# Performance work log

Measured on AMD Instinct MI355X. Metric: run time of the kernel, lower is better.

## Reference

```python
import jax, jax.numpy as jnp
import numpy as np

PAGE = 16  # page_size hard-coded in the torch module's forward


def setup_inputs() -> dict:
    rng = np.random.default_rng(0)
    B = 4096
    pre = rng.integers(0, 4096, size=B).astype(np.int32)
    ext = rng.integers(1, 8192, size=B).astype(np.int32)
    seq = (pre + ext).astype(np.int32)
    # last token slot of the existing prefix (identity layout); -1 when pre==0
    # (kernel never reads it in that case since num_part1 == 0).
    last_loc = (pre - 1).astype(np.int32)
    free_page = rng.permutation(2_097_152).astype(np.int32)
    return {
        "pre_lens": jnp.asarray(pre),
        "seq_lens": jnp.asarray(seq),
        "last_loc": jnp.asarray(last_loc),
        "free_page": jnp.asarray(free_page),
    }


def reference(pre_lens, seq_lens, last_loc, free_page):
    ext = seq_lens - pre_lens                      # [B] extend length per seq
    cum = jnp.cumsum(ext)                          # inclusive prefix sum
    starts = cum - ext                             # exclusive prefix sum = output_start_loc
    total = int(cum[-1])                           # total extend tokens (static given setup)

    pages_before = (pre_lens + PAGE - 1) // PAGE   # ceil(pre/page)
    pages_after = (seq_lens + PAGE - 1) // PAGE    # ceil(seq/page)
    new_pages = pages_after - pages_before
    new_start = jnp.cumsum(new_pages) - new_pages  # new_page_start_loc per seq

    # Per-token flat computation (replaces the per-program scatter):
    t = jnp.arange(total, dtype=jnp.int32)
    seg = jnp.searchsorted(cum, t, side="right").astype(jnp.int32)  # owning sequence
    o = t - starts[seg]                            # offset within this seq's extend
    p = pre_lens[seg] + o                          # absolute position in sequence

    # part1: tokens filling the existing partially-used page -> contiguous after last_loc
    boundary = pages_before[seg] * PAGE            # ceil(pre/page)*page
    in_part1 = p < boundary
    val1 = last_loc[seg] + 1 + o

    # part2/part3: tokens on newly allocated pages pulled from free_page
    k = p // PAGE - pages_before[seg]              # which new page (>=0 when not part1)
    idx = jnp.clip(new_start[seg] + k, 0, free_page.shape[0] - 1)
    val2 = free_page[idx] * PAGE + p % PAGE

    return jnp.where(in_part1, val1, val2).astype(jnp.int32)
```

## Files before the change

### kernel.cpp

```cpp
#include <hip/hip_runtime.h>

#define PAGE_SHIFT 4
#define PAGE_MASK 15
#define TOK_PER_BLOCK 1024
#define MAX_EXT_TILES 8

__global__ __launch_bounds__(1024) void scan_kernel(const int* __restrict__ pre_lens,
                                                    const int* __restrict__ seq_lens,
                                                    int B,
                                                    int* __restrict__ starts,
                                                    int* __restrict__ new_start) {
    __shared__ int w_e[16];
    __shared__ int w_n[16];
    const int t = threadIdx.x;
    const int lane = t & 63;
    const int wv = t >> 6;
    const int i0 = t * 4;

    int pe[4], se[4];
    if (i0 + 3 < B) {
        int4 pv = *reinterpret_cast<const int4*>(pre_lens + i0);
        int4 sv = *reinterpret_cast<const int4*>(seq_lens + i0);
        pe[0] = pv.x; pe[1] = pv.y; pe[2] = pv.z; pe[3] = pv.w;
        se[0] = sv.x; se[1] = sv.y; se[2] = sv.z; se[3] = sv.w;
    } else {
#pragma unroll
        for (int j = 0; j < 4; ++j) {
            pe[j] = (i0 + j < B) ? pre_lens[i0 + j] : 0;
            se[j] = (i0 + j < B) ? seq_lens[i0 + j] : 0;
        }
    }

    int e[4], np[4];
    int tot_e = 0, tot_n = 0;
#pragma unroll
    for (int j = 0; j < 4; ++j) {
        e[j] = se[j] - pe[j];
        int pb = (pe[j] + PAGE_MASK) >> PAGE_SHIFT;
        int pa = (se[j] + PAGE_MASK) >> PAGE_SHIFT;
        np[j] = pa - pb;
        tot_e += e[j];
        tot_n += np[j];
    }

    int sc_e = tot_e, sc_n = tot_n;
#pragma unroll
    for (int d = 1; d < 64; d <<= 1) {
        int ve = __shfl_up(sc_e, d, 64);
        int vn = __shfl_up(sc_n, d, 64);
        if (lane >= d) { sc_e += ve; sc_n += vn; }
    }
    if (lane == 63) { w_e[wv] = sc_e; w_n[wv] = sc_n; }
    __syncthreads();

    if (wv == 0) {
        int ve = (lane < 16) ? w_e[lane] : 0;
        int vn = (lane < 16) ? w_n[lane] : 0;
#pragma unroll
        for (int d = 1; d < 16; d <<= 1) {
            int ae = __shfl_up(ve, d, 64);
            int an = __shfl_up(vn, d, 64);
            if (lane >= d) { ve += ae; vn += an; }
        }
        if (lane < 16) { w_e[lane] = ve; w_n[lane] = vn; }
    }
    __syncthreads();

    int base_e = (wv > 0 ? w_e[wv - 1] : 0) + (sc_e - tot_e);
    int base_n = (wv > 0 ? w_n[wv - 1] : 0) + (sc_n - tot_n);

    if (i0 + 3 < B) {
        int4 oe, on;
        oe.x = base_e;            on.x = base_n;
        oe.y = oe.x + e[0];       on.y = on.x + np[0];
        oe.z = oe.y + e[1];       on.z = on.y + np[1];
        oe.w = oe.z + e[2];       on.w = on.z + np[2];
        *reinterpret_cast<int4*>(starts + i0) = oe;
        *reinterpret_cast<int4*>(new_start + i0) = on;
    } else {
#pragma unroll
        for (int j = 0; j < 4; ++j) {
            if (i0 + j < B) { starts[i0 + j] = base_e; new_start[i0 + j] = base_n; }
            base_e += e[j];
            base_n += np[j];
        }
    }
}

__device__ __forceinline__ int slot_value(int o, int pre, int boundary, int pb, int ll1,
                                          int ns, const int* __restrict__ fp, int n_free) {
    int p = pre + o;
    if (p < boundary) return ll1 + o;
    int idx = ns + (p >> PAGE_SHIFT) - pb;
    idx = min(max(idx, 0), n_free - 1);
    return fp[idx] * (1 << PAGE_SHIFT) + (p & PAGE_MASK);
}

__global__ __launch_bounds__(256) void assign_kernel(const int* __restrict__ pre_lens,
                                                     const int* __restrict__ seq_lens,
                                                     const int* __restrict__ last_loc,
                                                     const int* __restrict__ free_page,
                                                     const int* __restrict__ starts,
                                                     const int* __restrict__ new_start,
                                                     int* __restrict__ out,
                                                     int n_free) {
    const int b = blockIdx.x;
    const int pre = pre_lens[b];
    const int ext = seq_lens[b] - pre;
    const int start = starts[b];
    const int al = (-start) & 3;
    const int ty = blockIdx.y;

    for (int obase = al + ty * TOK_PER_BLOCK; ; obase += gridDim.y * TOK_PER_BLOCK) {
        bool any = (obase < ext) || (ty == 0 && obase == al);
        if (!any) return;

        const int ll1 = last_loc[b] + 1;
        const int pb = (pre + PAGE_MASK) >> PAGE_SHIFT;
        const int boundary = pb << PAGE_SHIFT;
        const int ns = new_start[b];

        if (ty == 0 && obase == al) {
            int o = (int)threadIdx.x;
            if (o < al && o < ext) {
                out[start + o] = slot_value(o, pre, boundary, pb, ll1, ns, free_page, n_free);
            }
        }

        int o = obase + (int)threadIdx.x * 4;
        if (o + 3 < ext) {
            int4 v;
            v.x = slot_value(o,     pre, boundary, pb, ll1, ns, free_page, n_free);
            v.y = slot_value(o + 1, pre, boundary, pb, ll1, ns, free_page, n_free);
            v.z = slot_value(o + 2, pre, boundary, pb, ll1, ns, free_page, n_free);
            v.w = slot_value(o + 3, pre, boundary, pb, ll1, ns, free_page, n_free);
            *reinterpret_cast<int4*>(out + start + o) = v;
        } else {
            for (int oo = o; oo < ext; ++oo) {
                out[start + oo] = slot_value(oo, pre, boundary, pb, ll1, ns, free_page, n_free);
            }
        }
        if (obase + gridDim.y * TOK_PER_BLOCK >= ext) return;
    }
}

extern "C" void kernel_launch(void* const* d_in, const int* in_sizes, int n_in,
                              void* d_out, int out_size, void* d_ws, size_t ws_size,
                              hipStream_t stream) {
    const int* pre_lens  = (const int*)d_in[0];
    const int* seq_lens  = (const int*)d_in[1];
    const int* last_loc  = (const int*)d_in[2];
    const int* free_page = (const int*)d_in[3];
    const int B = in_sizes[0];
    const int n_free = in_sizes[3];

    int* starts    = (int*)d_ws;
    int* new_start = ((int*)d_ws) + B;

    scan_kernel<<<1, 1024, 0, stream>>>(pre_lens, seq_lens, B, starts, new_start);
    dim3 grid(B, MAX_EXT_TILES);
    assign_kernel<<<grid, 256, 0, stream>>>(pre_lens, seq_lens, last_loc, free_page,
                                            starts, new_start, (int*)d_out, n_free);
}
```

Before: 102.3 us.

## Process 16 tokens per thread with two page lookups and shrink grid

Each thread now handles 16 consecutive tokens and loads at most two free_page entries (the current and next page) instead of one gather per token, then writes four int4 stores. The grid's y dimension drops from 8 to 2 tiles of 4096 tokens, so far fewer empty blocks launch and per-block setup loads are hoisted out of the loop. Fewer threads do more work each, which may cut latency hiding for long sequences.

```diff
diff --git a/kernel.cpp b/kernel.cpp
--- a/kernel.cpp
+++ b/kernel.cpp
@@ -2,8 +2,6 @@
 
 #define PAGE_SHIFT 4
 #define PAGE_MASK 15
-#define TOK_PER_BLOCK 1024
-#define MAX_EXT_TILES 8
 
 __global__ __launch_bounds__(1024) void scan_kernel(const int* __restrict__ pre_lens,
                                                     const int* __restrict__ seq_lens,
@@ -96,6 +94,9 @@
     return fp[idx] * (1 << PAGE_SHIFT) + (p & PAGE_MASK);
 }
 
+#define TOK_PER_THREAD 16
+#define TOK_PER_BLOCK (256 * TOK_PER_THREAD)
+
 __global__ __launch_bounds__(256) void assign_kernel(const int* __restrict__ pre_lens,
                                                      const int* __restrict__ seq_lens,
                                                      const int* __restrict__ last_loc,
@@ -110,37 +111,56 @@
     const int start = starts[b];
     const int al = (-start) & 3;
     const int ty = blockIdx.y;
+    const int ll1 = last_loc[b] + 1;
+    const int pb = (pre + PAGE_MASK) >> PAGE_SHIFT;
+    const int boundary = pb << PAGE_SHIFT;
+    const int ns = new_start[b];
 
-    for (int obase = al + ty * TOK_PER_BLOCK; ; obase += gridDim.y * TOK_PER_BLOCK) {
-        bool any = (obase < ext) || (ty == 0 && obase == al);
-        if (!any) return;
+    if (ty == 0) {
+        int t = (int)threadIdx.x;
+        if (t < al && t < ext) {
+            out[start + t] = slot_value(t, pre, boundary, pb, ll1, ns, free_page, n_free);
+        }
+    }
 
-        const int ll1 = last_loc[b] + 1;
-        const int pb = (pre + PAGE_MASK) >> PAGE_SHIFT;
-        const int boundary = pb << PAGE_SHIFT;
-        const int ns = new_start[b];
+    const int stride = (int)gridDim.y * TOK_PER_BLOCK;
+    for (int obase = al + ty * TOK_PER_BLOCK; obase < ext; obase += stride) {
+        const int o0 = obase + (int)threadIdx.x * TOK_PER_THREAD;
+        if (o0 >= ext) break;
 
-        if (ty == 0 && obase == al) {
-            int o = (int)threadIdx.x;
-            if (o < al && o < ext) {
+        const int p0 = pre + o0;
+        const int c = p0 & PAGE_MASK;
+        const int pageA = p0 >> PAGE_SHIFT;
+        int idxA = ns + pageA - pb;
+        int idxB = idxA + 1;
+        idxA = min(max(idxA, 0), n_free - 1);
+        idxB = min(max(idxB, 0), n_free - 1);
+        const int baseA = free_page[idxA] << PAGE_SHIFT;
+        const int baseB = free_page[idxB] << PAGE_SHIFT;
+        const bool p1A = pageA < pb;
+        const bool p1B = (pageA + 1) < pb;
+
+        if (o0 + TOK_PER_THREAD - 1 < ext) {
+            int vals[TOK_PER_THREAD];
+#pragma unroll
+            for (int j = 0; j < TOK_PER_THREAD; ++j) {
+                int cj = c + j;
+                bool inB = cj >= 16;
+                bool part1 = inB ? p1B : p1A;
+                int v2 = (inB ? baseB : baseA) + (cj & PAGE_MASK);
+                vals[j] = part1 ? (ll1 + o0 + j) : v2;
+            }
+            int4* dst = reinterpret_cast<int4*>(out + start + o0);
+#pragma unroll
+            for (int q = 0; q < 4; ++q) {
+                dst[q] = make_int4(vals[4 * q], vals[4 * q + 1],
+                                   vals[4 * q + 2], vals[4 * q + 3]);
+            }
+        } else {
+            for (int o = o0; o < ext; ++o) {
                 out[start + o] = slot_value(o, pre, boundary, pb, ll1, ns, free_page, n_free);
             }
         }
-
-        int o = obase + (int)threadIdx.x * 4;
-        if (o + 3 < ext) {
-            int4 v;
-            v.x = slot_value(o,     pre, boundary, pb, ll1, ns, free_page, n_free);
-            v.y = slot_value(o + 1, pre, boundary, pb, ll1, ns, free_page, n_free);
-            v.z = slot_value(o + 2, pre, boundary, pb, ll1, ns, free_page, n_free);
-            v.w = slot_value(o + 3, pre, boundary, pb, ll1, ns, free_page, n_free);
-            *reinterpret_cast<int4*>(out + start + o) = v;
-        } else {
-            for (int oo = o; oo < ext; ++oo) {
-                out[start + oo] = slot_value(oo, pre, boundary, pb, ll1, ns, free_page, n_free);
-            }
-        }
-        if (obase + gridDim.y * TOK_PER_BLOCK >= ext) return;
     }
 }
 
@@ -158,7 +178,7 @@
     int* new_start = ((int*)d_ws) + B;
 
     scan_kernel<<<1, 1024, 0, stream>>>(pre_lens, seq_lens, B, starts, new_start);
-    dim3 grid(B, MAX_EXT_TILES);
+    dim3 grid(B, 2);
     assign_kernel<<<grid, 256, 0, stream>>>(pre_lens, seq_lens, last_loc, free_page,
                                             starts, new_start, (int*)d_out, n_free);
 }
```

New measurement: 105.6 us. 3.3% more time.
